# Optimization experiments

Measured on AMD Instinct MI355X. Metric: run time of the kernel, lower is better.

## Reference

```python
import jax, jax.numpy as jnp
import numpy as np

K = 4096          # infeatures
N = 12288         # outfeatures
M = 4096          # tokens (batch*seq)
GROUPSIZE = 128
G = K // GROUPSIZE  # 32 groups
PACK = 8          # 8 int4 nibbles per int32


def _unpack_int4(q):
    """Unpack int32 [R, C] -> int32 [R, C*8]; nibble j of word c maps to column c*8+j."""
    shifts = jnp.arange(0, 32, 4, dtype=jnp.int32)          # [8]
    nib = (q[:, :, None] >> shifts[None, None, :]) & 0xF    # [R, C, 8]
    return nib.reshape(q.shape[0], -1)


def setup_inputs() -> dict:
    key = jax.random.key(0)
    k1, k2, k3, k4, k5 = jax.random.split(key, 5)
    x = jax.random.normal(k1, (M, K), dtype=jnp.float32)
    qweight = jax.random.randint(k2, (K, N // PACK), 0, 2147483647, dtype=jnp.int32)
    qzeros = jax.random.randint(k3, (G, N // PACK), 0, 2147483647, dtype=jnp.int32)
    scales = jax.random.uniform(k4, (G, N), dtype=jnp.float32, minval=0.001, maxval=0.01)
    bias = jax.random.normal(k5, (N,), dtype=jnp.float32)
    return {"x": x, "qweight": qweight, "qzeros": qzeros, "scales": scales,
            "bias": bias, "groupsize": GROUPSIZE}


def reference(x, qweight, qzeros, scales, bias, groupsize):
    # Dequantize: w[k, n] = (q4[k, n] - z4[k//gs, n]) * scales[k//gs, n]
    w_int = _unpack_int4(qweight)                 # [K, N] int32, values 0..15
    z_int = _unpack_int4(qzeros)                  # [G, N] int32 (+1 already folded in)
    z_full = jnp.repeat(z_int, groupsize, axis=0)      # [K, N]
    s_full = jnp.repeat(scales, groupsize, axis=0)     # [K, N]
    weight = (w_int - z_full).astype(x.dtype) * s_full  # [K, N]
    out = x @ weight + bias                        # [M, N]
    return out
```

## Files before the change

kernel.cpp:

```cpp
#include <hip/hip_runtime.h>

#define M_DIM 4096
#define N_DIM 12288
#define K_DIM 4096
#define NP    1536
#define GS    128

typedef unsigned short ushort_t;
typedef _Float16 half8 __attribute__((ext_vector_type(8)));
typedef unsigned short us8 __attribute__((ext_vector_type(8)));
typedef float f32x16 __attribute__((ext_vector_type(16)));

__device__ __forceinline__ unsigned short f2h(float f) {
  _Float16 h = (_Float16)f;
  return __builtin_bit_cast(unsigned short, h);
}

#define GLDS16(G, L) __builtin_amdgcn_global_load_lds(                      \
    (const __attribute__((address_space(1))) void*)(G),                     \
    (__attribute__((address_space(3))) void*)(L), 16, 0, 0)

#define DQ_BLOCKS (96 * 64)
#define CVT_BLOCKS (M_DIM * K_DIM / 8 / 256)

__global__ __launch_bounds__(256) void prep_kernel(
    const int* __restrict__ qw, const int* __restrict__ qz,
    const float* __restrict__ sc, ushort_t* __restrict__ wt,
    const float* __restrict__ x, ushort_t* __restrict__ xb) {
  __shared__ int ldsQ[64 * 16];
  __shared__ int ldsZ[16];
  const int tid = threadIdx.x;
  if (blockIdx.x >= DQ_BLOCKS) {
    int cid = (blockIdx.x - DQ_BLOCKS) * 256 + tid;
    const float4* p = (const float4*)(x + (size_t)cid * 8);
    float4 a = p[0], b = p[1];
    us8 o;
    o[0] = f2h(a.x); o[1] = f2h(a.y); o[2] = f2h(a.z); o[3] = f2h(a.w);
    o[4] = f2h(b.x); o[5] = f2h(b.y); o[6] = f2h(b.z); o[7] = f2h(b.w);
    *(us8*)(xb + (size_t)cid * 8) = o;
    return;
  }
  const int bx = blockIdx.x % 96;
  const int by = blockIdx.x / 96;
  const int k0 = by * 64;
  const int n0 = bx * 128;
  const int w0 = n0 >> 3;
  const int g  = k0 >> 7;
#pragma unroll
  for (int i = 0; i < 4; ++i) {
    int idx = i * 256 + tid;
    int row = idx >> 4, w = idx & 15;
    ldsQ[row * 16 + (w ^ (row & 15))] = qw[(size_t)(k0 + row) * NP + w0 + w];
  }
  if (tid < 16) ldsZ[tid] = qz[g * NP + w0 + tid];
  __syncthreads();
  const int nl  = tid >> 1;
  const int kh  = tid & 1;
  const int col = nl >> 3;
  const int j4  = (nl & 7) * 4;
  const int z   = (ldsZ[col] >> j4) & 0xF;
  const float s = sc[(size_t)g * N_DIM + n0 + nl];
  ushort_t* dst = wt + (size_t)(n0 + nl) * K_DIM + k0 + kh * 32;
#pragma unroll
  for (int c = 0; c < 4; ++c) {
    us8 o;
#pragma unroll
    for (int ii = 0; ii < 8; ++ii) {
      int row = kh * 32 + c * 8 + ii;
      int q = (ldsQ[row * 16 + (col ^ (row & 15))] >> j4) & 0xF;
      o[ii] = f2h((float)(q - z) * s);
    }
    *(us8*)(dst + c * 8) = o;
  }
}

template <int APRE, int BPRE>
__global__ __launch_bounds__(256) void gemm_kernel(
    const ushort_t* __restrict__ Xb, const float* __restrict__ Xf,
    const ushort_t* __restrict__ Wt,
    const int* __restrict__ qw, const int* __restrict__ qz,
    const float* __restrict__ sc,
    const float* __restrict__ bias, float* __restrict__ out) {
  __shared__ __align__(16) ushort_t lsA[128 * 64];
  __shared__ __align__(16) ushort_t lsB[128 * 64];
  const int tid  = threadIdx.x;
  const int lane = tid & 63;
  const int wid  = tid >> 6;
  const int wm   = wid & 1;
  const int wn   = wid >> 1;
  const int m0   = blockIdx.x * 128;
  const int n0   = blockIdx.y * 128;

  f32x16 acc[2][2] = {};

  for (int kt = 0; kt < K_DIM / 64; ++kt) {
    const int kb = kt * 64;
    if constexpr (APRE) {
#pragma unroll
      for (int i = 0; i < 4; ++i) {
        int cid = i * 256 + tid;
        int r = cid >> 3, scol = cid & 7;
        int c = scol ^ (r & 7);
        GLDS16(Xb + (size_t)(m0 + r) * K_DIM + kb + c * 8, lsA + cid * 8);
      }
    } else {
#pragma unroll
      for (int i = 0; i < 4; ++i) {
        int cid = i * 256 + tid;
        int r = cid >> 3, scol = cid & 7;
        int c = scol ^ (r & 7);
        const float* src = Xf + (size_t)(m0 + r) * K_DIM + kb + c * 8;
        float4 a = *(const float4*)src;
        float4 b = *(const float4*)(src + 4);
        us8 o;
        o[0] = f2h(a.x); o[1] = f2h(a.y); o[2] = f2h(a.z); o[3] = f2h(a.w);
        o[4] = f2h(b.x); o[5] = f2h(b.y); o[6] = f2h(b.z); o[7] = f2h(b.w);
        *(us8*)(lsA + cid * 8) = o;
      }
    }
    if constexpr (BPRE) {
#pragma unroll
      for (int i = 0; i < 4; ++i) {
        int cid = i * 256 + tid;
        int r = cid >> 3, scol = cid & 7;
        int c = scol ^ (r & 7);
        GLDS16(Wt + (size_t)(n0 + r) * K_DIM + kb + c * 8, lsB + cid * 8);
      }
    } else {
#pragma unroll
      for (int i = 0; i < 4; ++i) {
        int wi = i * 256 + tid;
        int kl = wi >> 4, cw = wi & 15;
        int k = kb + kl;
        int g = k >> 7;
        int qword = qw[(size_t)k * NP + (n0 >> 3) + cw];
        int zword = qz[g * NP + (n0 >> 3) + cw];
        float4 s0 = *(const float4*)(sc + (size_t)g * N_DIM + n0 + cw * 8);
        float4 s1 = *(const float4*)(sc + (size_t)g * N_DIM + n0 + cw * 8 + 4);
        float sv[8] = {s0.x, s0.y, s0.z, s0.w, s1.x, s1.y, s1.z, s1.w};
#pragma unroll
        for (int j = 0; j < 8; ++j) {
          int nl = cw * 8 + j;
          int q = (qword >> (4 * j)) & 0xF;
          int z = (zword >> (4 * j)) & 0xF;
          lsB[nl * 64 + (((kl >> 3) ^ (nl & 7)) << 3) + (kl & 7)] =
              f2h((float)(q - z) * sv[j]);
        }
      }
    }
    __syncthreads();
#pragma unroll
    for (int ks = 0; ks < 4; ++ks) {
      half8 af[2], bfr[2];
      const int h = lane >> 5;
      const int c = ks * 2 + h;
#pragma unroll
      for (int i = 0; i < 2; ++i) {
        int row = wm * 64 + i * 32 + (lane & 31);
        af[i] = *(const half8*)(lsA + (row * 8 + (c ^ (row & 7))) * 8);
      }
#pragma unroll
      for (int jj = 0; jj < 2; ++jj) {
        int row = wn * 64 + jj * 32 + (lane & 31);
        bfr[jj] = *(const half8*)(lsB + (row * 8 + (c ^ (row & 7))) * 8);
      }
#pragma unroll
      for (int i = 0; i < 2; ++i)
#pragma unroll
        for (int jj = 0; jj < 2; ++jj)
          acc[i][jj] = __builtin_amdgcn_mfma_f32_32x32x16_f16(
              af[i], bfr[jj], acc[i][jj], 0, 0, 0);
    }
    __syncthreads();
  }

#pragma unroll
  for (int jj = 0; jj < 2; ++jj) {
    int n = n0 + wn * 64 + jj * 32 + (lane & 31);
    float bv = bias[n];
#pragma unroll
    for (int i = 0; i < 2; ++i) {
      int mbase = m0 + wm * 64 + i * 32 + ((lane >> 5) << 2);
#pragma unroll
      for (int reg = 0; reg < 16; ++reg) {
        int m = mbase + (reg & 3) + ((reg >> 2) << 3);
        __builtin_nontemporal_store(acc[i][jj][reg] + bv,
                                    out + (size_t)m * N_DIM + n);
      }
    }
  }
}

extern "C" void kernel_launch(void* const* d_in, const int* in_sizes, int n_in,
                              void* d_out, int out_size, void* d_ws, size_t ws_size,
                              hipStream_t stream) {
  const float* x    = (const float*)d_in[0];
  const int*   qw   = (const int*)d_in[1];
  const int*   qz   = (const int*)d_in[2];
  const float* sc   = (const float*)d_in[3];
  const float* bias = (const float*)d_in[4];
  float*       out  = (float*)d_out;

  const size_t WT_BYTES = (size_t)N_DIM * K_DIM * 2;
  const size_t XB_BYTES = (size_t)M_DIM * K_DIM * 2;
  ushort_t* Wt = (ushort_t*)d_ws;
  ushort_t* Xb = (ushort_t*)((char*)d_ws + WT_BYTES);
  const bool hasWt = ws_size >= WT_BYTES;
  const bool hasXb = ws_size >= WT_BYTES + XB_BYTES;

  dim3 grid(M_DIM / 128, N_DIM / 128);
  if (hasXb) {
    prep_kernel<<<DQ_BLOCKS + CVT_BLOCKS, 256, 0, stream>>>(qw, qz, sc, Wt, x, Xb);
    gemm_kernel<1, 1><<<grid, 256, 0, stream>>>(Xb, x, Wt, qw, qz, sc, bias, out);
  } else if (hasWt) {
    prep_kernel<<<DQ_BLOCKS, 256, 0, stream>>>(qw, qz, sc, Wt, x, nullptr);
    gemm_kernel<0, 1><<<grid, 256, 0, stream>>>(nullptr, x, Wt, qw, qz, sc, bias, out);
  } else {
    gemm_kernel<0, 0><<<grid, 256, 0, stream>>>(nullptr, x, nullptr, qw, qz, sc, bias, out);
  }
}
```

Before: 707.3 us.

## Add 256x256-tile multi-stage pipelined GEMM kernel with 16x16x32 MFMA

Replaces the 128x128 single-buffered GEMM with a 512-thread 256x256 tile kernel that stages 32-wide K slices through a double-buffered 128KB LDS ring using global_load_lds, prefetching three units ahead with explicit vmcnt waits and barriers. It switches to 16x16x32 MFMA with 8x4 accumulators per wave and raises wave priority around the MFMA block. This targets the exposed load latency and barrier stalls of the old kernel and raises arithmetic intensity per tile. In exchange it uses much more LDS and registers, which lowers occupancy, and relies on hand-placed waitcnt counts being correct.

```diff
diff --git a/kernel.cpp b/kernel.cpp
--- a/kernel.cpp
+++ b/kernel.cpp
@@ -10,6 +10,7 @@
 typedef _Float16 half8 __attribute__((ext_vector_type(8)));
 typedef unsigned short us8 __attribute__((ext_vector_type(8)));
 typedef float f32x16 __attribute__((ext_vector_type(16)));
+typedef float f32x4 __attribute__((ext_vector_type(4)));
 
 __device__ __forceinline__ unsigned short f2h(float f) {
   _Float16 h = (_Float16)f;
@@ -74,6 +75,111 @@
   }
 }
 
+
+__device__ __forceinline__ void stage_unit(
+    int u, const ushort_t* __restrict__ Ag, const ushort_t* __restrict__ Bg,
+    int m0, int n0, int tid, ushort_t* lds) {
+  const int t   = u >> 1;
+  const int ks  = u & 1;
+  const int b   = t & 1;
+  const int kbu = t * 64 + ks * 32;
+  const int r   = tid >> 1;
+  const int hp  = (tid & 1) ^ ((tid >> 3) & 1);
+  const size_t ka = (size_t)kbu + hp * 8;
+  ushort_t* dA = lds + b * 32768 + (2 * ks) * 4096 + tid * 8;
+  ushort_t* dB = dA + 16384;
+  const ushort_t* sA = Ag + (size_t)(m0 + r) * K_DIM + ka;
+  const ushort_t* sB = Bg + (size_t)(n0 + r) * K_DIM + ka;
+  GLDS16(sA,      dA);
+  GLDS16(sA + 16, dA + 4096);
+  GLDS16(sB,      dB);
+  GLDS16(sB + 16, dB + 4096);
+}
+
+template <int VN, bool STG>
+__device__ __forceinline__ void gemm_phase(
+    int p, const ushort_t* __restrict__ Ag, const ushort_t* __restrict__ Bg,
+    int m0, int n0, int tid, ushort_t* lds, f32x4 (&acc)[8][4]) {
+  const int lane = tid & 63;
+  const int wid  = tid >> 6;
+  const int wm   = wid & 1;
+  const int wn   = wid >> 1;
+  const int ks   = p & 1;
+  const int b    = (p >> 1) & 1;
+  const int c  = lane >> 4;
+  const int rl = lane & 15;
+  const int sg = (c & 1) ^ ((rl >> 2) & 1);
+  const ushort_t* base = lds + b * 32768 + (2 * ks + (c >> 1)) * 4096 + sg * 8;
+  const ushort_t* pa = base + (wm * 128 + rl) * 16;
+  const ushort_t* pb = base + 16384 + (wn * 64 + rl) * 16;
+  half8 af[8], bf[4];
+#pragma unroll
+  for (int i = 0; i < 8; ++i) af[i] = *(const half8*)(pa + i * 256);
+#pragma unroll
+  for (int j = 0; j < 4; ++j) bf[j] = *(const half8*)(pb + j * 256);
+  if constexpr (STG) stage_unit(p + 3, Ag, Bg, m0, n0, tid, lds);
+  __builtin_amdgcn_s_barrier();
+  asm volatile("s_waitcnt lgkmcnt(0)" ::: "memory");
+  __builtin_amdgcn_sched_barrier(0);
+  __builtin_amdgcn_s_setprio(1);
+#pragma unroll
+  for (int i = 0; i < 8; ++i)
+#pragma unroll
+    for (int j = 0; j < 4; ++j)
+      acc[i][j] = __builtin_amdgcn_mfma_f32_16x16x32_f16(af[i], bf[j],
+                                                         acc[i][j], 0, 0, 0);
+  __builtin_amdgcn_s_setprio(0);
+  if constexpr (VN == 8)      asm volatile("s_waitcnt vmcnt(8)" ::: "memory");
+  else if constexpr (VN == 4) asm volatile("s_waitcnt vmcnt(4)" ::: "memory");
+  else if constexpr (VN == 0) asm volatile("s_waitcnt vmcnt(0)" ::: "memory");
+  if constexpr (VN >= 0) {
+    __builtin_amdgcn_s_barrier();
+    asm volatile("" ::: "memory");
+  }
+}
+
+__global__ __launch_bounds__(512, 2) void gemm256_kernel(
+    const ushort_t* __restrict__ Xb, const ushort_t* __restrict__ Wt,
+    const float* __restrict__ bias, float* __restrict__ out) {
+  __shared__ __align__(16) ushort_t lds[65536];
+  const int tid = threadIdx.x;
+  const int m0  = blockIdx.x * 256;
+  const int n0  = blockIdx.y * 256;
+  f32x4 acc[8][4] = {};
+
+  stage_unit(0, Xb, Wt, m0, n0, tid, lds);
+  stage_unit(1, Xb, Wt, m0, n0, tid, lds);
+  stage_unit(2, Xb, Wt, m0, n0, tid, lds);
+  asm volatile("s_waitcnt vmcnt(8)" ::: "memory");
+  __builtin_amdgcn_s_barrier();
+  asm volatile("" ::: "memory");
+
+#pragma unroll 4
+  for (int p = 0; p < 124; ++p)
+    gemm_phase<8, true>(p, Xb, Wt, m0, n0, tid, lds, acc);
+  gemm_phase<8, true >(124, Xb, Wt, m0, n0, tid, lds, acc);
+  gemm_phase<4, false>(125, Xb, Wt, m0, n0, tid, lds, acc);
+  gemm_phase<0, false>(126, Xb, Wt, m0, n0, tid, lds, acc);
+  gemm_phase<-1, false>(127, Xb, Wt, m0, n0, tid, lds, acc);
+
+  const int lane = tid & 63;
+  const int wm   = (tid >> 6) & 1;
+  const int wn   = tid >> 7;
+#pragma unroll
+  for (int jj = 0; jj < 4; ++jj) {
+    int n = n0 + wn * 64 + jj * 16 + (lane & 15);
+    float bv = bias[n];
+#pragma unroll
+    for (int i = 0; i < 8; ++i) {
+      int mb = (int)(m0 + wm * 128 + i * 16 + ((lane >> 4) << 2));
+#pragma unroll
+      for (int r = 0; r < 4; ++r)
+        __builtin_nontemporal_store(acc[i][jj][r] + bv,
+                                    out + (size_t)(mb + r) * N_DIM + n);
+    }
+  }
+}
+
 template <int APRE, int BPRE>
 __global__ __launch_bounds__(256) void gemm_kernel(
     const ushort_t* __restrict__ Xb, const float* __restrict__ Xf,
@@ -208,14 +314,16 @@
   const bool hasWt = ws_size >= WT_BYTES;
   const bool hasXb = ws_size >= WT_BYTES + XB_BYTES;
 
-  dim3 grid(M_DIM / 128, N_DIM / 128);
   if (hasXb) {
     prep_kernel<<<DQ_BLOCKS + CVT_BLOCKS, 256, 0, stream>>>(qw, qz, sc, Wt, x, Xb);
-    gemm_kernel<1, 1><<<grid, 256, 0, stream>>>(Xb, x, Wt, qw, qz, sc, bias, out);
+    dim3 grid256(M_DIM / 256, N_DIM / 256);
+    gemm256_kernel<<<grid256, 512, 0, stream>>>(Xb, Wt, bias, out);
   } else if (hasWt) {
+    dim3 grid(M_DIM / 128, N_DIM / 128);
     prep_kernel<<<DQ_BLOCKS, 256, 0, stream>>>(qw, qz, sc, Wt, x, nullptr);
     gemm_kernel<0, 1><<<grid, 256, 0, stream>>>(nullptr, x, Wt, qw, qz, sc, bias, out);
   } else {
+    dim3 grid(M_DIM / 128, N_DIM / 128);
     gemm_kernel<0, 0><<<grid, 256, 0, stream>>>(nullptr, x, nullptr, qw, qz, sc, bias, out);
   }
 }
```

Result: faster. 668.7 us (-5.5%).

## Add 256x256 tiled GEMM with triple-buffered LDS staging and register double-buffering

Applied to the files above, without the earlier changes.

Replaces the 128x128 GEMM on the prepared-workspace path with a 256x256-tile, 512-thread kernel. It stages K-slices into LDS several units ahead with global_load_lds, double-buffers MFMA operand fragments in registers, and places explicit waitcnt, sched_barrier and setprio calls so loads overlap MFMA work. The prep kernel also loads qweight with 128-bit vector loads. This targets the per-tile load stalls and two-barrier-per-iteration structure of the old kernel, in exchange for 128 KB of LDS per block, higher register pressure and hand-tuned counter waits that are fragile if miscounted.

```diff
diff --git a/kernel.cpp b/kernel.cpp
--- a/kernel.cpp
+++ b/kernel.cpp
@@ -10,6 +10,7 @@
 typedef _Float16 half8 __attribute__((ext_vector_type(8)));
 typedef unsigned short us8 __attribute__((ext_vector_type(8)));
 typedef float f32x16 __attribute__((ext_vector_type(16)));
+typedef float f32x4 __attribute__((ext_vector_type(4)));
 
 __device__ __forceinline__ unsigned short f2h(float f) {
   _Float16 h = (_Float16)f;
@@ -31,13 +32,13 @@
   __shared__ int ldsZ[16];
   const int tid = threadIdx.x;
   if (blockIdx.x >= DQ_BLOCKS) {
-    int cid = (blockIdx.x - DQ_BLOCKS) * 256 + tid;
-    const float4* p = (const float4*)(x + (size_t)cid * 8);
+    size_t cid = (size_t)(blockIdx.x - DQ_BLOCKS) * 256 + tid;
+    const float4* p = (const float4*)(x + cid * 8);
     float4 a = p[0], b = p[1];
     us8 o;
     o[0] = f2h(a.x); o[1] = f2h(a.y); o[2] = f2h(a.z); o[3] = f2h(a.w);
     o[4] = f2h(b.x); o[5] = f2h(b.y); o[6] = f2h(b.z); o[7] = f2h(b.w);
-    *(us8*)(xb + (size_t)cid * 8) = o;
+    *(us8*)(xb + cid * 8) = o;
     return;
   }
   const int bx = blockIdx.x % 96;
@@ -46,11 +47,13 @@
   const int n0 = bx * 128;
   const int w0 = n0 >> 3;
   const int g  = k0 >> 7;
-#pragma unroll
-  for (int i = 0; i < 4; ++i) {
-    int idx = i * 256 + tid;
-    int row = idx >> 4, w = idx & 15;
-    ldsQ[row * 16 + (w ^ (row & 15))] = qw[(size_t)(k0 + row) * NP + w0 + w];
+  {
+    int row = tid >> 2, qc = tid & 3;
+    int4 v = *(const int4*)(qw + (size_t)(k0 + row) * NP + w0 + qc * 4);
+    ldsQ[row * 16 + ((qc * 4 + 0) ^ (row & 15))] = v.x;
+    ldsQ[row * 16 + ((qc * 4 + 1) ^ (row & 15))] = v.y;
+    ldsQ[row * 16 + ((qc * 4 + 2) ^ (row & 15))] = v.z;
+    ldsQ[row * 16 + ((qc * 4 + 3) ^ (row & 15))] = v.w;
   }
   if (tid < 16) ldsZ[tid] = qz[g * NP + w0 + tid];
   __syncthreads();
@@ -71,6 +74,147 @@
       o[ii] = f2h((float)(q - z) * s);
     }
     *(us8*)(dst + c * 8) = o;
+  }
+}
+
+
+__device__ __forceinline__ void stage_unit(
+    int u, const ushort_t* __restrict__ Ag, const ushort_t* __restrict__ Bg,
+    int m0, int n0, int tid, ushort_t* lds) {
+  const int b   = (u >> 1) & 1;
+  const int ks  = u & 1;
+  const int kbu = (u >> 1) * 64 + ks * 32;
+  const int r   = tid >> 1;
+  const int hp  = (tid & 1) ^ ((tid >> 3) & 1);
+  const size_t ka = (size_t)kbu + hp * 8;
+  ushort_t* dA = lds + b * 32768 + (2 * ks) * 4096 + tid * 8;
+  ushort_t* dB = dA + 16384;
+  const ushort_t* sA = Ag + (size_t)(m0 + r) * K_DIM + ka;
+  const ushort_t* sB = Bg + (size_t)(n0 + r) * K_DIM + ka;
+  GLDS16(sA,      dA);
+  GLDS16(sA + 16, dA + 4096);
+  GLDS16(sB,      dB);
+  GLDS16(sB + 16, dB + 4096);
+}
+
+#define SB() __builtin_amdgcn_sched_barrier(0)
+
+#define MFMA8(A, B)                                                           \
+  do {                                                                        \
+    acc[0][0] = __builtin_amdgcn_mfma_f32_32x32x16_f16(A[0], B[0], acc[0][0], 0, 0, 0); \
+    acc[0][1] = __builtin_amdgcn_mfma_f32_32x32x16_f16(A[0], B[1], acc[0][1], 0, 0, 0); \
+    acc[1][0] = __builtin_amdgcn_mfma_f32_32x32x16_f16(A[1], B[0], acc[1][0], 0, 0, 0); \
+    acc[1][1] = __builtin_amdgcn_mfma_f32_32x32x16_f16(A[1], B[1], acc[1][1], 0, 0, 0); \
+    acc[2][0] = __builtin_amdgcn_mfma_f32_32x32x16_f16(A[2], B[0], acc[2][0], 0, 0, 0); \
+    acc[2][1] = __builtin_amdgcn_mfma_f32_32x32x16_f16(A[2], B[1], acc[2][1], 0, 0, 0); \
+    acc[3][0] = __builtin_amdgcn_mfma_f32_32x32x16_f16(A[3], B[0], acc[3][0], 0, 0, 0); \
+    acc[3][1] = __builtin_amdgcn_mfma_f32_32x32x16_f16(A[3], B[1], acc[3][1], 0, 0, 0); \
+  } while (0)
+
+#define LOAD_SET(A, B, sbase)                                                 \
+  do {                                                                        \
+    const ushort_t* A_ = pa + (sbase);                                        \
+    const ushort_t* B_ = pb + (sbase);                                        \
+    A[0] = *(const half8*)(A_);                                               \
+    A[1] = *(const half8*)(A_ + 512);                                         \
+    A[2] = *(const half8*)(A_ + 1024);                                        \
+    A[3] = *(const half8*)(A_ + 1536);                                        \
+    B[0] = *(const half8*)(B_);                                               \
+    B[1] = *(const half8*)(B_ + 512);                                         \
+  } while (0)
+
+template <bool STG, int VN, bool LOAD2>
+__device__ __forceinline__ void gemm_phase(
+    int q, const ushort_t* __restrict__ Ag, const ushort_t* __restrict__ Bg,
+    int m0, int n0, int tid, ushort_t* lds,
+    const ushort_t* pa, const ushort_t* pb,
+    half8 (&a0)[4], half8 (&b0)[2], half8 (&a1)[4], half8 (&b1)[2],
+    f32x16 (&acc)[4][2]) {
+  if constexpr (STG) stage_unit(q + 3, Ag, Bg, m0, n0, tid, lds);
+  {
+    const int sb = ((q & 2) << 14) + ((q & 1) << 13) + 4096;
+    LOAD_SET(a1, b1, sb);
+  }
+  SB();
+  asm volatile("s_waitcnt lgkmcnt(6)" ::: "memory");
+  SB();
+  __builtin_amdgcn_s_setprio(1);
+  MFMA8(a0, b0);
+  __builtin_amdgcn_s_setprio(0);
+  SB();
+  if constexpr (LOAD2) {
+    const int u = q + 1;
+    const int sb = ((u & 2) << 14) + ((u & 1) << 13);
+    LOAD_SET(a0, b0, sb);
+    SB();
+    asm volatile("s_waitcnt lgkmcnt(6)" ::: "memory");
+  } else {
+    asm volatile("s_waitcnt lgkmcnt(0)" ::: "memory");
+  }
+  SB();
+  __builtin_amdgcn_s_setprio(1);
+  MFMA8(a1, b1);
+  __builtin_amdgcn_s_setprio(0);
+  SB();
+  if constexpr (VN == 4)      asm volatile("s_waitcnt vmcnt(4)" ::: "memory");
+  else if constexpr (VN == 0) asm volatile("s_waitcnt vmcnt(0)" ::: "memory");
+  if constexpr (VN >= 0) {
+    __builtin_amdgcn_s_barrier();
+    asm volatile("" ::: "memory");
+  }
+}
+
+__global__ __launch_bounds__(512, 2) void gemm256_kernel(
+    const ushort_t* __restrict__ Xb, const ushort_t* __restrict__ Wt,
+    const float* __restrict__ bias, float* __restrict__ out) {
+  __shared__ __align__(16) ushort_t lds[65536];
+  const int tid  = threadIdx.x;
+  const int lane = tid & 63;
+  const int wid  = tid >> 6;
+  const int wm   = wid & 1;
+  const int wn   = wid >> 1;
+  const int m0   = blockIdx.x * 256;
+  const int n0   = blockIdx.y * 256;
+  f32x16 acc[4][2] = {};
+
+  const int loff = (lane & 31) * 16 + (((lane >> 5) ^ ((lane >> 2) & 1)) << 3);
+  const ushort_t* pa = lds + loff + wm * 2048;
+  const ushort_t* pb = lds + loff + 16384 + wn * 1024;
+
+  half8 a0[4], b0[2], a1[4], b1[2];
+
+  stage_unit(0, Xb, Wt, m0, n0, tid, lds);
+  stage_unit(1, Xb, Wt, m0, n0, tid, lds);
+  stage_unit(2, Xb, Wt, m0, n0, tid, lds);
+  asm volatile("s_waitcnt vmcnt(4)" ::: "memory");
+  __builtin_amdgcn_s_barrier();
+  asm volatile("" ::: "memory");
+  LOAD_SET(a0, b0, 0);
+  SB();
+
+#pragma unroll 4
+  for (int q = 0; q < 124; ++q)
+    gemm_phase<true, 4, true>(q, Xb, Wt, m0, n0, tid, lds, pa, pb,
+                              a0, b0, a1, b1, acc);
+  gemm_phase<true,  4, true >(124, Xb, Wt, m0, n0, tid, lds, pa, pb, a0, b0, a1, b1, acc);
+  gemm_phase<false, 0, true >(125, Xb, Wt, m0, n0, tid, lds, pa, pb, a0, b0, a1, b1, acc);
+  gemm_phase<false, -2, true>(126, Xb, Wt, m0, n0, tid, lds, pa, pb, a0, b0, a1, b1, acc);
+  gemm_phase<false, -2, false>(127, Xb, Wt, m0, n0, tid, lds, pa, pb, a0, b0, a1, b1, acc);
+
+#pragma unroll
+  for (int jj = 0; jj < 2; ++jj) {
+    int n = n0 + wn * 64 + jj * 32 + (lane & 31);
+    float bv = bias[n];
+#pragma unroll
+    for (int i = 0; i < 4; ++i) {
+      int mbase = m0 + wm * 128 + i * 32 + ((lane >> 5) << 2);
+#pragma unroll
+      for (int reg = 0; reg < 16; ++reg) {
+        int m = mbase + (reg & 3) + ((reg >> 2) << 3);
+        __builtin_nontemporal_store(acc[i][jj][reg] + bv,
+                                    out + (size_t)m * N_DIM + n);
+      }
+    }
   }
 }
 
@@ -208,14 +352,16 @@
   const bool hasWt = ws_size >= WT_BYTES;
   const bool hasXb = ws_size >= WT_BYTES + XB_BYTES;
 
-  dim3 grid(M_DIM / 128, N_DIM / 128);
   if (hasXb) {
     prep_kernel<<<DQ_BLOCKS + CVT_BLOCKS, 256, 0, stream>>>(qw, qz, sc, Wt, x, Xb);
-    gemm_kernel<1, 1><<<grid, 256, 0, stream>>>(Xb, x, Wt, qw, qz, sc, bias, out);
+    dim3 grid256(M_DIM / 256, N_DIM / 256);
+    gemm256_kernel<<<grid256, 512, 0, stream>>>(Xb, Wt, bias, out);
   } else if (hasWt) {
+    dim3 grid(M_DIM / 128, N_DIM / 128);
     prep_kernel<<<DQ_BLOCKS, 256, 0, stream>>>(qw, qz, sc, Wt, x, nullptr);
     gemm_kernel<0, 1><<<grid, 256, 0, stream>>>(nullptr, x, Wt, qw, qz, sc, bias, out);
   } else {
+    dim3 grid(M_DIM / 128, N_DIM / 128);
     gemm_kernel<0, 0><<<grid, 256, 0, stream>>>(nullptr, x, nullptr, qw, qz, sc, bias, out);
   }
 }
```

Measured after the change: 682.2 us. 1.04x faster.
